# Optimization experiments

Measured on AMD Instinct MI355X. Metric: run time of the kernel, lower is better.

## Reference

```python
import jax, jax.numpy as jnp
import numpy as np

B, L, D = 32, 256, 128


def hard_sigmoid(x):
    # Keras-1 default inner_activation for LSTM gates
    return jnp.clip(0.2 * x + 0.5, 0.0, 1.0)


def lstm_step(x_t, h, c, W, U, b):
    # Keras-1 gate order: i, f, c(candidate), o
    z = x_t @ W + h @ U + b  # [B, 4D]
    d = h.shape[-1]
    i = hard_sigmoid(z[:, :d])
    f = hard_sigmoid(z[:, d:2 * d])
    g = jnp.tanh(z[:, 2 * d:3 * d])
    o = hard_sigmoid(z[:, 3 * d:])
    c_new = f * c + i * g
    h_new = o * jnp.tanh(c_new)
    return h_new, c_new


def setup_inputs() -> dict:
    key = jax.random.key(0)
    ks = jax.random.split(key, 9)
    s = 0.05  # weight scale to keep activations in a sane range
    return {
        "x": jax.random.normal(ks[0], (B, L, D), dtype=jnp.float32),
        "Wr": jax.random.normal(ks[1], (D, 4 * D), dtype=jnp.float32) * s,
        "Ur": jax.random.normal(ks[2], (D, 4 * D), dtype=jnp.float32) * s,
        "br": jnp.zeros((4 * D,), dtype=jnp.float32),
        "Ww": jax.random.normal(ks[3], (D, 4 * D), dtype=jnp.float32) * s,
        "Uw": jax.random.normal(ks[4], (D, 4 * D), dtype=jnp.float32) * s,
        "bw": jnp.zeros((4 * D,), dtype=jnp.float32),
        "Wc": jax.random.normal(ks[5], (2 * D, D), dtype=jnp.float32) * s,
        "bc": jnp.zeros((D,), dtype=jnp.float32),
    }


def reference(x, Wr, Ur, br, Ww, Uw, bw, Wc, bc):
    b, l, d = x.shape
    h0 = jnp.zeros((b, d), dtype=x.dtype)

    # ---- reader LSTM (return_sequences) ----
    def reader_step(carry, x_t):
        h, c = carry
        h, c = lstm_step(x_t, h, c, Wr, Ur, br)
        return (h, c), h

    _, o_seq = jax.lax.scan(reader_step, (h0, h0), jnp.swapaxes(x, 0, 1))  # [L, B, D]

    # ---- compose-and-write scan over timesteps ----
    mem0 = x  # read() sets mem_0 = input

    def write_step(carry, o_t):
        mem, h, c = carry  # mem: [B, L, D]
        # eq 2-3: attention over memory slots
        z = jax.nn.softmax(jnp.einsum('bd,bld->bl', o_t, mem), axis=-1)  # [B, L]
        m_rt = jnp.einsum('bl,bld->bd', z, mem)  # [B, D]
        # eq 4: composer (linear activation)
        c_t = jnp.concatenate([o_t, m_rt], axis=-1) @ Wc + bc  # [B, D]
        # eq 5: writer LSTM step
        h, c = lstm_step(c_t, h, c, Ww, Uw, bw)
        # eq 6: soft overwrite of memory
        zc = z[:, :, None]
        mem = mem * (1.0 - zc) + h[:, None, :] * zc
        return (mem, h, c), h

    (_, _, _), hs = jax.lax.scan(write_step, (mem0, h0, h0), o_seq)
    # return_mode == 'last_output'
    return hs[-1]
```

## Files before the change

### kernel.cpp

```cpp
#include <hip/hip_runtime.h>
#include <stdint.h>


#define LL 256

typedef float v2f __attribute__((ext_vector_type(2)));

__device__ __forceinline__ float hsig(float x) { return fminf(fmaxf(fmaf(x, 0.2f, 0.5f), 0.f), 1.f); }
__device__ __forceinline__ float tanh_fast(float x) {
  x = fminf(fmaxf(x, -15.f), 15.f);
  float e = __expf(2.f * x);
  return (e - 1.f) / (e + 1.f);
}

__global__ __launch_bounds__(512) void wtrans_kernel(const float* __restrict__ src,
                                                     float* __restrict__ dst, int jshift) {
  int idx = blockIdx.x * 512 + threadIdx.x;
  int J = 1 << jshift;
  int k = idx >> jshift, j = idx & (J - 1);
  dst[(((size_t)(k >> 2) << jshift) + j) * 4 + (k & 3)] = src[idx];
}

__global__ __launch_bounds__(512) void xw_gemm(const float* __restrict__ x,
                                               const float4* __restrict__ WrT4,
                                               const float* __restrict__ br,
                                               float* __restrict__ XW) {
  alignas(16) __shared__ float xs[8][128];
  const int b = blockIdx.x >> 5, tg = blockIdx.x & 31, tid = threadIdx.x;
  const float* xg = x + ((size_t)b * LL + tg * 8) * 128;
  if (tid < 256) ((float4*)&xs[0][0])[tid] = ((const float4*)xg)[tid];
  __syncthreads();
  float acc[8];
#pragma unroll
  for (int r = 0; r < 8; r++) acc[r] = 0.f;
#pragma unroll 8
  for (int i4 = 0; i4 < 32; i4++) {
    float4 w4 = WrT4[i4 * 512 + tid];
#pragma unroll
    for (int r = 0; r < 8; r++) {
      float4 v = *(const float4*)&xs[r][4 * i4];
      acc[r] += w4.x * v.x + w4.y * v.y + w4.z * v.z + w4.w * v.w;
    }
  }
  const float brj = br[tid];
  float* o = XW + ((size_t)b * LL + tg * 8) * 512;
#pragma unroll
  for (int r = 0; r < 8; r++) o[r * 512 + tid] = acc[r] + brj;
}

__global__ __launch_bounds__(512) void owc_gemm(const float* __restrict__ og,
                                                const float4* __restrict__ WcT4,
                                                const float* __restrict__ bc,
                                                float* __restrict__ OWc) {
  alignas(16) __shared__ float os[8][128];
  const int b = blockIdx.x >> 5, tg = blockIdx.x & 31, tid = threadIdx.x;
  const int j = tid & 127, r2 = tid >> 7;
  const float* g = og + ((size_t)b * LL + tg * 8) * 128;
  if (tid < 256) ((float4*)&os[0][0])[tid] = ((const float4*)g)[tid];
  __syncthreads();
  float a0 = 0.f, a1 = 0.f;
#pragma unroll 8
  for (int i4 = 0; i4 < 32; i4++) {
    float4 w4 = WcT4[i4 * 128 + j];
    float4 v0 = *(const float4*)&os[r2 * 2][4 * i4];
    float4 v1 = *(const float4*)&os[r2 * 2 + 1][4 * i4];
    a0 += w4.x * v0.x + w4.y * v0.y + w4.z * v0.z + w4.w * v0.w;
    a1 += w4.x * v1.x + w4.y * v1.y + w4.z * v1.z + w4.w * v1.w;
  }
  const float bcj = bc[j];
  float* o = OWc + ((size_t)b * LL + tg * 8) * 128;
  o[(r2 * 2) * 128 + j] = a0 + bcj;
  o[(r2 * 2 + 1) * 128 + j] = a1 + bcj;
}

__global__ __launch_bounds__(512, 2) void reader_kernel(const float4* __restrict__ UrT4,
                                                        const float* __restrict__ XW,
                                                        float* __restrict__ og) {
  alignas(16) __shared__ float h_s[128];
  alignas(16) __shared__ float pp_s[512];
  const int b = blockIdx.x, tid = threadIdx.x;
  const float* XWb = XW + (size_t)b * LL * 512;
  float* ogb = og + (size_t)b * LL * 128;

  float4 U[32];
#pragma unroll
  for (int i4 = 0; i4 < 32; i4++) U[i4] = UrT4[i4 * 512 + tid];

  float c_r = 0.f;
  if (tid < 128) h_s[tid] = 0.f;
  float xwv = XWb[tid];
  __syncthreads();

  for (int t = 0; t < LL; t++) {
    float xw_n = (t + 1 < LL) ? XWb[(t + 1) * 512 + tid] : 0.f;
    v2f acc[4] = {{0.f, 0.f}, {0.f, 0.f}, {0.f, 0.f}, {0.f, 0.f}};
#pragma unroll
    for (int i4 = 0; i4 < 32; i4++) {
      float4 v = *(const float4*)&h_s[4 * i4];
      float4 w = U[i4];
      acc[i4 & 3] += (v2f){w.x, w.y} * (v2f){v.x, v.y};
      acc[i4 & 3] += (v2f){w.z, w.w} * (v2f){v.z, v.w};
    }
    v2f A = (acc[0] + acc[1]) + (acc[2] + acc[3]);
    pp_s[tid] = A.x + A.y + xwv;
    __syncthreads();
    if (tid < 128) {
      float zi = pp_s[tid], zf = pp_s[128 + tid], zg = pp_s[256 + tid], zo = pp_s[384 + tid];
      float ii = hsig(zi), ff = hsig(zf), gg = tanh_fast(zg), oo = hsig(zo);
      c_r = fmaf(ff, c_r, ii * gg);
      float h = oo * tanh_fast(c_r);
      h_s[tid] = h;
      ogb[t * 128 + tid] = h;
    }
    __syncthreads();
    xwv = xw_n;
  }
}

__global__ __launch_bounds__(512, 2) void writer_kernel(
    const float* __restrict__ x,
    const float4* __restrict__ WwT4, const float4* __restrict__ UwT4,
    const float4* __restrict__ WcT4,
    const float* __restrict__ bw,
    const float* __restrict__ og, const float* __restrict__ OWc,
    float* __restrict__ out) {
  alignas(16) __shared__ float h_s[128];
  alignas(16) __shared__ float osN[128];
  alignas(16) __shared__ float ow_s[128];
  alignas(16) __shared__ float sc_s[256], ee_s[256];
  alignas(16) __shared__ float mr_s[128], ct_s[128];
  alignas(16) __shared__ float pp_s[1024];
  __shared__ float rr_s[16];

  const int b = blockIdx.x, tid = threadIdx.x;
  const int lane = tid & 63, wv = tid >> 6;
  const int l = tid >> 1, hf = tid & 1;
  const int q = tid >> 6, dp = tid & 63;
  const int jj = tid & 127, kq = tid >> 7;

  const float* xg = x + (size_t)b * (LL * 128);
  const float* ogb = og + (size_t)b * (LL * 128);
  const float* owb = OWc + (size_t)b * (LL * 128);

  v2f Mr[32], Mc[32];
#pragma unroll
  for (int w = 0; w < 32; w++) Mr[w] = *(const v2f*)(xg + l * 128 + hf * 64 + 2 * w);
#pragma unroll
  for (int i = 0; i < 32; i++) Mc[i] = *(const v2f*)(xg + (q * 32 + i) * 128 + 2 * dp);

  const float bwj = bw[tid];

  float c_w = 0.f;
  if (tid < 128) { h_s[tid] = 0.f; osN[tid] = ogb[tid]; }
  __syncthreads();
  {
    v2f S = {0.f, 0.f};
#pragma unroll
    for (int w = 0; w < 32; w++) S += Mr[w] * (*(const v2f*)&osN[hf * 64 + 2 * w]);
    float s = S.x + S.y;
    s += __shfl_xor(s, 1);
    if (hf == 0) sc_s[l] = s;
  }
  __syncthreads();

  for (int t = 0; t < LL; t++) {
    if (tid >= 128 && tid < 256) {
      if (t + 1 < LL) osN[tid - 128] = ogb[(t + 1) * 128 + (tid - 128)];
    } else if (tid >= 256 && tid < 384) {
      ow_s[tid - 256] = owb[t * 128 + (tid - 256)];
    }
    if (tid < 256) {
      float m = sc_s[tid];
#pragma unroll
      for (int off = 32; off > 0; off >>= 1) m = fmaxf(m, __shfl_xor(m, off));
      if (lane == 0) rr_s[wv] = m;
    }
    __syncthreads();
    if (tid < 256) {
      float mx = fmaxf(fmaxf(rr_s[0], rr_s[1]), fmaxf(rr_s[2], rr_s[3]));
      float e = __expf(sc_s[tid] - mx);
      ee_s[tid] = e;
      float s2 = e;
#pragma unroll
      for (int off = 32; off > 0; off >>= 1) s2 += __shfl_xor(s2, off);
      if (lane == 0) rr_s[8 + wv] = s2;
    }
    __syncthreads();
    const float inv = 1.f / (rr_s[8] + rr_s[9] + rr_s[10] + rr_s[11]);
    {
      v2f P = {0.f, 0.f};
#pragma unroll
      for (int i = 0; i < 32; i++) P += Mc[i] * ee_s[q * 32 + i];
      *(v2f*)&pp_s[q * 128 + 2 * dp] = P;
    }
    __syncthreads();
    if (tid < 128) {
      float s = 0.f;
#pragma unroll
      for (int g = 0; g < 8; g++) s += pp_s[g * 128 + tid];
      mr_s[tid] = s * inv;
    }
    __syncthreads();
    {
      v2f A = {0.f, 0.f};
#pragma unroll 4
      for (int i8 = 0; i8 < 8; i8++) {
        float4 w4 = WcT4[(size_t)(32 + kq * 8 + i8) * 128 + jj];
        float4 v4 = *(const float4*)&mr_s[kq * 32 + 4 * i8];
        A += (v2f){w4.x, w4.y} * (v2f){v4.x, v4.y};
        A += (v2f){w4.z, w4.w} * (v2f){v4.z, v4.w};
      }
      pp_s[kq * 128 + jj] = A.x + A.y;
    }
    __syncthreads();
    if (tid < 128)
      ct_s[tid] = ow_s[tid] + pp_s[tid] + pp_s[128 + tid] + pp_s[256 + tid] + pp_s[384 + tid];
    __syncthreads();
    {
      v2f a0 = {0.f, 0.f}, a1 = {0.f, 0.f}, a2 = {0.f, 0.f}, a3 = {0.f, 0.f};
#pragma unroll 2
      for (int o = 0; o < 8; o++) {
        float4 w0 = WwT4[(o * 4 + 0) * 512 + tid]; float4 x0 = *(const float4*)&ct_s[16 * o + 0];
        float4 w1 = WwT4[(o * 4 + 1) * 512 + tid]; float4 x1 = *(const float4*)&ct_s[16 * o + 4];
        float4 w2 = WwT4[(o * 4 + 2) * 512 + tid]; float4 x2 = *(const float4*)&ct_s[16 * o + 8];
        float4 w3 = WwT4[(o * 4 + 3) * 512 + tid]; float4 x3 = *(const float4*)&ct_s[16 * o + 12];
        a0 += (v2f){w0.x, w0.y} * (v2f){x0.x, x0.y}; a0 += (v2f){w0.z, w0.w} * (v2f){x0.z, x0.w};
        a1 += (v2f){w1.x, w1.y} * (v2f){x1.x, x1.y}; a1 += (v2f){w1.z, w1.w} * (v2f){x1.z, x1.w};
        a2 += (v2f){w2.x, w2.y} * (v2f){x2.x, x2.y}; a2 += (v2f){w2.z, w2.w} * (v2f){x2.z, x2.w};
        a3 += (v2f){w3.x, w3.y} * (v2f){x3.x, x3.y}; a3 += (v2f){w3.z, w3.w} * (v2f){x3.z, x3.w};
      }
#pragma unroll 2
      for (int o = 0; o < 8; o++) {
        float4 w0 = UwT4[(o * 4 + 0) * 512 + tid]; float4 x0 = *(const float4*)&h_s[16 * o + 0];
        float4 w1 = UwT4[(o * 4 + 1) * 512 + tid]; float4 x1 = *(const float4*)&h_s[16 * o + 4];
        float4 w2 = UwT4[(o * 4 + 2) * 512 + tid]; float4 x2 = *(const float4*)&h_s[16 * o + 8];
        float4 w3 = UwT4[(o * 4 + 3) * 512 + tid]; float4 x3 = *(const float4*)&h_s[16 * o + 12];
        a0 += (v2f){w0.x, w0.y} * (v2f){x0.x, x0.y}; a0 += (v2f){w0.z, w0.w} * (v2f){x0.z, x0.w};
        a1 += (v2f){w1.x, w1.y} * (v2f){x1.x, x1.y}; a1 += (v2f){w1.z, w1.w} * (v2f){x1.z, x1.w};
        a2 += (v2f){w2.x, w2.y} * (v2f){x2.x, x2.y}; a2 += (v2f){w2.z, w2.w} * (v2f){x2.z, x2.w};
        a3 += (v2f){w3.x, w3.y} * (v2f){x3.x, x3.y}; a3 += (v2f){w3.z, w3.w} * (v2f){x3.z, x3.w};
      }
      v2f A = (a0 + a1) + (a2 + a3);
      pp_s[tid] = A.x + A.y + bwj;
    }
    __syncthreads();
    if (tid < 128) {
      float zi = pp_s[tid], zf = pp_s[128 + tid], zg = pp_s[256 + tid], zo = pp_s[384 + tid];
      float ii = hsig(zi), ff = hsig(zf), gg = tanh_fast(zg), oo = hsig(zo);
      c_w = fmaf(ff, c_w, ii * gg);
      h_s[tid] = oo * tanh_fast(c_w);
    }
    __syncthreads();
    if (t + 1 < LL) {
      const float zr = ee_s[l] * inv;
      v2f S = {0.f, 0.f};
#pragma unroll
      for (int w = 0; w < 32; w++) {
        v2f h2 = *(const v2f*)&h_s[hf * 64 + 2 * w];
        v2f m = Mr[w];
        v2f n = m + (h2 - m) * zr;
        Mr[w] = n;
        S += n * (*(const v2f*)&osN[hf * 64 + 2 * w]);
      }
      float s = S.x + S.y;
      s += __shfl_xor(s, 1);
      if (hf == 0) sc_s[l] = s;
      v2f hc = *(const v2f*)&h_s[2 * dp];
#pragma unroll
      for (int i = 0; i < 32; i++) {
        float zc = ee_s[q * 32 + i] * inv;
        v2f m = Mc[i];
        Mc[i] = m + (hc - m) * zc;
      }
    }
    __syncthreads();
  }

  if (tid < 128) out[b * 128 + tid] = h_s[tid];
}

extern "C" void kernel_launch(void* const* d_in, const int* in_sizes, int n_in,
                              void* d_out, int out_size, void* d_ws, size_t ws_size,
                              hipStream_t stream) {
  const float* x  = (const float*)d_in[0];
  const float* Wr = (const float*)d_in[1];
  const float* Ur = (const float*)d_in[2];
  const float* br = (const float*)d_in[3];
  const float* Ww = (const float*)d_in[4];
  const float* Uw = (const float*)d_in[5];
  const float* bw = (const float*)d_in[6];
  const float* Wc = (const float*)d_in[7];
  const float* bc = (const float*)d_in[8];
  float* out = (float*)d_out;

  float* og  = (float*)d_ws;
  float* XW  = og + 1048576;
  float* OWc = XW + 4194304;
  float* WrT = OWc + 1048576;
  float* UrT = WrT + 65536;
  float* WwT = UrT + 65536;
  float* UwT = WwT + 65536;
  float* WcT = UwT + 65536;

  wtrans_kernel<<<128, 512, 0, stream>>>(Wr, WrT, 9);
  wtrans_kernel<<<128, 512, 0, stream>>>(Ur, UrT, 9);
  wtrans_kernel<<<128, 512, 0, stream>>>(Ww, WwT, 9);
  wtrans_kernel<<<128, 512, 0, stream>>>(Uw, UwT, 9);
  wtrans_kernel<<<64, 512, 0, stream>>>(Wc, WcT, 7);
  xw_gemm<<<1024, 512, 0, stream>>>(x, (const float4*)WrT, br, XW);
  reader_kernel<<<32, 512, 0, stream>>>((const float4*)UrT, XW, og);
  owc_gemm<<<1024, 512, 0, stream>>>(og, (const float4*)WcT, bc, OWc);
  writer_kernel<<<32, 512, 0, stream>>>(x, (const float4*)WwT, (const float4*)UwT,
                                        (const float4*)WcT, bw, og, OWc, out);
}
```

Measured before the change: 2.166 ms.

## Fold composer weights into writer LSTM input weights and cache Uw in LDS

```diff
diff --git a/kernel.cpp b/kernel.cpp
--- a/kernel.cpp
+++ b/kernel.cpp
@@ -19,6 +19,33 @@
   int J = 1 << jshift;
   int k = idx >> jshift, j = idx & (J - 1);
   dst[(((size_t)(k >> 2) << jshift) + j) * 4 + (k & 3)] = src[idx];
+}
+
+__global__ __launch_bounds__(512) void pvw_gemm(const float* __restrict__ Wc,
+                                                const float* __restrict__ Ww,
+                                                float* __restrict__ PVw) {
+  __shared__ float wrow[128];
+  const int r = blockIdx.x, j = threadIdx.x;
+  if (j < 128) wrow[j] = Wc[r * 128 + j];
+  __syncthreads();
+  float a = 0.f;
+#pragma unroll 4
+  for (int m = 0; m < 128; m++) a = fmaf(wrow[m], Ww[m * 512 + j], a);
+  PVw[r * 512 + j] = a;
+}
+
+__global__ __launch_bounds__(512) void pz_kernel(const float* __restrict__ bc,
+                                                 const float* __restrict__ Ww,
+                                                 const float* __restrict__ bw,
+                                                 float* __restrict__ pz) {
+  __shared__ float b_s[128];
+  const int j = threadIdx.x;
+  if (j < 128) b_s[j] = bc[j];
+  __syncthreads();
+  float a = bw[j];
+#pragma unroll 4
+  for (int m = 0; m < 128; m++) a = fmaf(b_s[m], Ww[m * 512 + j], a);
+  pz[j] = a;
 }
 
 __global__ __launch_bounds__(512) void xw_gemm(const float* __restrict__ x,
@@ -48,31 +75,6 @@
   for (int r = 0; r < 8; r++) o[r * 512 + tid] = acc[r] + brj;
 }
 
-__global__ __launch_bounds__(512) void owc_gemm(const float* __restrict__ og,
-                                                const float4* __restrict__ WcT4,
-                                                const float* __restrict__ bc,
-                                                float* __restrict__ OWc) {
-  alignas(16) __shared__ float os[8][128];
-  const int b = blockIdx.x >> 5, tg = blockIdx.x & 31, tid = threadIdx.x;
-  const int j = tid & 127, r2 = tid >> 7;
-  const float* g = og + ((size_t)b * LL + tg * 8) * 128;
-  if (tid < 256) ((float4*)&os[0][0])[tid] = ((const float4*)g)[tid];
-  __syncthreads();
-  float a0 = 0.f, a1 = 0.f;
-#pragma unroll 8
-  for (int i4 = 0; i4 < 32; i4++) {
-    float4 w4 = WcT4[i4 * 128 + j];
-    float4 v0 = *(const float4*)&os[r2 * 2][4 * i4];
-    float4 v1 = *(const float4*)&os[r2 * 2 + 1][4 * i4];
-    a0 += w4.x * v0.x + w4.y * v0.y + w4.z * v0.z + w4.w * v0.w;
-    a1 += w4.x * v1.x + w4.y * v1.y + w4.z * v1.z + w4.w * v1.w;
-  }
-  const float bcj = bc[j];
-  float* o = OWc + ((size_t)b * LL + tg * 8) * 128;
-  o[(r2 * 2) * 128 + j] = a0 + bcj;
-  o[(r2 * 2 + 1) * 128 + j] = a1 + bcj;
-}
-
 __global__ __launch_bounds__(512, 2) void reader_kernel(const float4* __restrict__ UrT4,
                                                         const float* __restrict__ XW,
                                                         float* __restrict__ og) {
@@ -119,36 +121,33 @@
 
 __global__ __launch_bounds__(512, 2) void writer_kernel(
     const float* __restrict__ x,
-    const float4* __restrict__ WwT4, const float4* __restrict__ UwT4,
-    const float4* __restrict__ WcT4,
-    const float* __restrict__ bw,
-    const float* __restrict__ og, const float* __restrict__ OWc,
-    float* __restrict__ out) {
+    const float4* __restrict__ VwT4, const float4* __restrict__ UwT4,
+    const float* __restrict__ og, const float* __restrict__ ZW,
+    float* __restrict__ out, const int NC) {
   alignas(16) __shared__ float h_s[128];
   alignas(16) __shared__ float osN[128];
-  alignas(16) __shared__ float ow_s[128];
   alignas(16) __shared__ float sc_s[256], ee_s[256];
-  alignas(16) __shared__ float mr_s[128], ct_s[128];
+  alignas(16) __shared__ float mr_s[128];
   alignas(16) __shared__ float pp_s[1024];
   __shared__ float rr_s[16];
+  extern __shared__ float4 UwL[];
 
   const int b = blockIdx.x, tid = threadIdx.x;
   const int lane = tid & 63, wv = tid >> 6;
   const int l = tid >> 1, hf = tid & 1;
   const int q = tid >> 6, dp = tid & 63;
-  const int jj = tid & 127, kq = tid >> 7;
 
   const float* xg = x + (size_t)b * (LL * 128);
   const float* ogb = og + (size_t)b * (LL * 128);
-  const float* owb = OWc + (size_t)b * (LL * 128);
+  const float* ZWb = ZW + (size_t)b * (LL * 512);
+
+  for (int i = tid; i < NC * 512; i += 512) UwL[i] = UwT4[i];
 
   v2f Mr[32], Mc[32];
 #pragma unroll
   for (int w = 0; w < 32; w++) Mr[w] = *(const v2f*)(xg + l * 128 + hf * 64 + 2 * w);
 #pragma unroll
   for (int i = 0; i < 32; i++) Mc[i] = *(const v2f*)(xg + (q * 32 + i) * 128 + 2 * dp);
-
-  const float bwj = bw[tid];
 
   float c_w = 0.f;
   if (tid < 128) { h_s[tid] = 0.f; osN[tid] = ogb[tid]; }
@@ -164,11 +163,9 @@
   __syncthreads();
 
   for (int t = 0; t < LL; t++) {
-    if (tid >= 128 && tid < 256) {
-      if (t + 1 < LL) osN[tid - 128] = ogb[(t + 1) * 128 + (tid - 128)];
-    } else if (tid >= 256 && tid < 384) {
-      ow_s[tid - 256] = owb[t * 128 + (tid - 256)];
-    }
+    float zwv = ZWb[(size_t)t * 512 + tid];
+    if (tid >= 128 && tid < 256 && t + 1 < LL)
+      osN[tid - 128] = ogb[(t + 1) * 128 + (tid - 128)];
     if (tid < 256) {
       float m = sc_s[tid];
 #pragma unroll
@@ -202,46 +199,42 @@
     }
     __syncthreads();
     {
-      v2f A = {0.f, 0.f};
-#pragma unroll 4
-      for (int i8 = 0; i8 < 8; i8++) {
-        float4 w4 = WcT4[(size_t)(32 + kq * 8 + i8) * 128 + jj];
-        float4 v4 = *(const float4*)&mr_s[kq * 32 + 4 * i8];
-        A += (v2f){w4.x, w4.y} * (v2f){v4.x, v4.y};
-        A += (v2f){w4.z, w4.w} * (v2f){v4.z, v4.w};
-      }
-      pp_s[kq * 128 + jj] = A.x + A.y;
-    }
-    __syncthreads();
-    if (tid < 128)
-      ct_s[tid] = ow_s[tid] + pp_s[tid] + pp_s[128 + tid] + pp_s[256 + tid] + pp_s[384 + tid];
-    __syncthreads();
-    {
       v2f a0 = {0.f, 0.f}, a1 = {0.f, 0.f}, a2 = {0.f, 0.f}, a3 = {0.f, 0.f};
 #pragma unroll 2
-      for (int o = 0; o < 8; o++) {
-        float4 w0 = WwT4[(o * 4 + 0) * 512 + tid]; float4 x0 = *(const float4*)&ct_s[16 * o + 0];
-        float4 w1 = WwT4[(o * 4 + 1) * 512 + tid]; float4 x1 = *(const float4*)&ct_s[16 * o + 4];
-        float4 w2 = WwT4[(o * 4 + 2) * 512 + tid]; float4 x2 = *(const float4*)&ct_s[16 * o + 8];
-        float4 w3 = WwT4[(o * 4 + 3) * 512 + tid]; float4 x3 = *(const float4*)&ct_s[16 * o + 12];
-        a0 += (v2f){w0.x, w0.y} * (v2f){x0.x, x0.y}; a0 += (v2f){w0.z, w0.w} * (v2f){x0.z, x0.w};
-        a1 += (v2f){w1.x, w1.y} * (v2f){x1.x, x1.y}; a1 += (v2f){w1.z, w1.w} * (v2f){x1.z, x1.w};
-        a2 += (v2f){w2.x, w2.y} * (v2f){x2.x, x2.y}; a2 += (v2f){w2.z, w2.w} * (v2f){x2.z, x2.w};
-        a3 += (v2f){w3.x, w3.y} * (v2f){x3.x, x3.y}; a3 += (v2f){w3.z, w3.w} * (v2f){x3.z, x3.w};
+      for (int i4 = 0; i4 < 32; i4 += 2) {
+        float4 w0 = VwT4[i4 * 512 + tid];
+        float4 w1 = VwT4[(i4 + 1) * 512 + tid];
+        float4 v0 = *(const float4*)&mr_s[4 * i4];
+        float4 v1 = *(const float4*)&mr_s[4 * i4 + 4];
+        a0 += (v2f){w0.x, w0.y} * (v2f){v0.x, v0.y};
+        a0 += (v2f){w0.z, w0.w} * (v2f){v0.z, v0.w};
+        a1 += (v2f){w1.x, w1.y} * (v2f){v1.x, v1.y};
+        a1 += (v2f){w1.z, w1.w} * (v2f){v1.z, v1.w};
       }
 #pragma unroll 2
-      for (int o = 0; o < 8; o++) {
-        float4 w0 = UwT4[(o * 4 + 0) * 512 + tid]; float4 x0 = *(const float4*)&h_s[16 * o + 0];
-        float4 w1 = UwT4[(o * 4 + 1) * 512 + tid]; float4 x1 = *(const float4*)&h_s[16 * o + 4];
-        float4 w2 = UwT4[(o * 4 + 2) * 512 + tid]; float4 x2 = *(const float4*)&h_s[16 * o + 8];
-        float4 w3 = UwT4[(o * 4 + 3) * 512 + tid]; float4 x3 = *(const float4*)&h_s[16 * o + 12];
-        a0 += (v2f){w0.x, w0.y} * (v2f){x0.x, x0.y}; a0 += (v2f){w0.z, w0.w} * (v2f){x0.z, x0.w};
-        a1 += (v2f){w1.x, w1.y} * (v2f){x1.x, x1.y}; a1 += (v2f){w1.z, w1.w} * (v2f){x1.z, x1.w};
-        a2 += (v2f){w2.x, w2.y} * (v2f){x2.x, x2.y}; a2 += (v2f){w2.z, w2.w} * (v2f){x2.z, x2.w};
-        a3 += (v2f){w3.x, w3.y} * (v2f){x3.x, x3.y}; a3 += (v2f){w3.z, w3.w} * (v2f){x3.z, x3.w};
-      }
-      v2f A = (a0 + a1) + (a2 + a3);
-      pp_s[tid] = A.x + A.y + bwj;
+      for (int i4 = 0; i4 < NC; i4 += 2) {
+        float4 w0 = UwL[i4 * 512 + tid];
+        float4 w1 = UwL[(i4 + 1) * 512 + tid];
+        float4 v0 = *(const float4*)&h_s[4 * i4];
+        float4 v1 = *(const float4*)&h_s[4 * i4 + 4];
+        a2 += (v2f){w0.x, w0.y} * (v2f){v0.x, v0.y};
+        a2 += (v2f){w0.z, w0.w} * (v2f){v0.z, v0.w};
+        a3 += (v2f){w1.x, w1.y} * (v2f){v1.x, v1.y};
+        a3 += (v2f){w1.z, w1.w} * (v2f){v1.z, v1.w};
+      }
+#pragma unroll 2
+      for (int i4 = NC; i4 < 32; i4 += 2) {
+        float4 w0 = UwT4[i4 * 512 + tid];
+        float4 w1 = UwT4[(i4 + 1) * 512 + tid];
+        float4 v0 = *(const float4*)&h_s[4 * i4];
+        float4 v1 = *(const float4*)&h_s[4 * i4 + 4];
+        a0 += (v2f){w0.x, w0.y} * (v2f){v0.x, v0.y};
+        a0 += (v2f){w0.z, w0.w} * (v2f){v0.z, v0.w};
+        a1 += (v2f){w1.x, w1.y} * (v2f){v1.x, v1.y};
+        a1 += (v2f){w1.z, w1.w} * (v2f){v1.z, v1.w};
+      }
+      v2f A = (a0 + a2) + (a1 + a3);
+      pp_s[tid] = A.x + A.y + zwv;
     }
     __syncthreads();
     if (tid < 128) {
@@ -295,21 +288,36 @@
 
   float* og  = (float*)d_ws;
   float* XW  = og + 1048576;
-  float* OWc = XW + 4194304;
-  float* WrT = OWc + 1048576;
+  float* WrT = XW + 4194304;
   float* UrT = WrT + 65536;
-  float* WwT = UrT + 65536;
-  float* UwT = WwT + 65536;
-  float* WcT = UwT + 65536;
+  float* UwT = UrT + 65536;
+  float* PVw = UwT + 65536;
+  float* PwT = PVw + 131072;
+  float* VwT = PwT + 65536;
+  float* pz  = VwT + 65536;
+
+  static int nc_cached = -1;
+  if (nc_cached < 0) {
+    int want = 18 * 512 * (int)sizeof(float4);
+    nc_cached = (hipFuncSetAttribute((const void*)writer_kernel,
+                                     hipFuncAttributeMaxDynamicSharedMemorySize,
+                                     want) == hipSuccess)
+                    ? 18
+                    : 6;
+  }
+  const int NC = nc_cached;
+  const size_t shbytes = (size_t)NC * 512 * sizeof(float4);
 
   wtrans_kernel<<<128, 512, 0, stream>>>(Wr, WrT, 9);
   wtrans_kernel<<<128, 512, 0, stream>>>(Ur, UrT, 9);
-  wtrans_kernel<<<128, 512, 0, stream>>>(Ww, WwT, 9);
   wtrans_kernel<<<128, 512, 0, stream>>>(Uw, UwT, 9);
-  wtrans_kernel<<<64, 512, 0, stream>>>(Wc, WcT, 7);
+  pvw_gemm<<<256, 512, 0, stream>>>(Wc, Ww, PVw);
+  pz_kernel<<<1, 512, 0, stream>>>(bc, Ww, bw, pz);
+  wtrans_kernel<<<128, 512, 0, stream>>>(PVw, PwT, 9);
+  wtrans_kernel<<<128, 512, 0, stream>>>(PVw + 65536, VwT, 9);
   xw_gemm<<<1024, 512, 0, stream>>>(x, (const float4*)WrT, br, XW);
   reader_kernel<<<32, 512, 0, stream>>>((const float4*)UrT, XW, og);
-  owc_gemm<<<1024, 512, 0, stream>>>(og, (const float4*)WcT, bc, OWc);
-  writer_kernel<<<32, 512, 0, stream>>>(x, (const float4*)WwT, (const float4*)UwT,
-                                        (const float4*)WcT, bw, og, OWc, out);
-}
+  xw_gemm<<<1024, 512, 0, stream>>>(og, (const float4*)PwT, pz, XW);
+  writer_kernel<<<32, 512, shbytes, stream>>>(x, (const float4*)VwT,
+                                              (const float4*)UwT, og, XW, out, NC);
+}
```

Result: faster. 1.905 ms (-12.0%).
